# Kernel optimization log

Hardware: AMD Instinct MI355X
Metric: run time of the kernel (lower is better)

Reference implementation:

```python
import jax, jax.numpy as jnp
import numpy as np

N, E = 100000, 1600000
IN, HID, EMB = 128, 256, 64


def setup_inputs() -> dict:
    key = jax.random.key(0)
    ks = jax.random.split(key, 8)
    x = jax.random.normal(ks[0], (N, IN), dtype=jnp.float32)
    edge_index = jax.random.randint(ks[1], (2, E), 0, N, dtype=jnp.int64)
    def glorot(k, fan_in, fan_out):
        lim = np.sqrt(6.0 / (fan_in + fan_out)).astype(np.float32)
        return jax.random.uniform(k, (fan_in, fan_out), jnp.float32, -lim, lim)
    return {
        "x": x,
        "edge_index": edge_index,
        "W1": glorot(ks[2], IN, HID), "b1": jnp.zeros((HID,), jnp.float32),
        "W2": glorot(ks[3], HID, HID), "b2": jnp.zeros((HID,), jnp.float32),
        "W3": glorot(ks[4], HID, EMB), "b3": jnp.zeros((EMB,), jnp.float32),
    }


def reference(x, edge_index, W1, b1, W2, b2, W3, b3):
    n = x.shape[0]
    # add self loops (PyG GCNConv default, fill_value=1)
    loops = jnp.arange(n, dtype=edge_index.dtype)
    src = jnp.concatenate([edge_index[0], loops])
    dst = jnp.concatenate([edge_index[1], loops])
    # symmetric normalization D^-1/2 A_hat D^-1/2 (degree at target)
    deg = jax.ops.segment_sum(jnp.ones_like(src, dtype=x.dtype), dst, num_segments=n)
    dinv = jnp.where(deg > 0, deg ** -0.5, 0.0)
    norm = (dinv[src] * dinv[dst])[:, None]  # [E+N, 1]

    def conv(h, W, b):
        h = h @ W                               # [N, out]
        agg = jax.ops.segment_sum(h[src] * norm, dst, num_segments=n)
        return agg + b

    h = jax.nn.relu(conv(x, W1, b1))   # dropout: identity in eval mode
    h = jax.nn.relu(conv(h, W2, b2))
    h = conv(h, W3, b3)
    # L2-normalize rows (F.normalize, eps=1e-12)
    nrm = jnp.linalg.norm(h, axis=1, keepdims=True)
    return h / jnp.maximum(nrm, 1e-12)
```

## Files before the change

### kernel.cpp

```cpp
#include <hip/hip_runtime.h>
#include <cstddef>
#include <cstdint>

constexpr int IN_F  = 128;
constexpr int HID_F = 256;
constexpr int EMB_F = 64;

typedef float  f32x4  __attribute__((ext_vector_type(4)));
typedef short  bf16x8 __attribute__((ext_vector_type(8)));
typedef unsigned short ushort_t;
typedef ushort_t u16x8 __attribute__((ext_vector_type(8)));
typedef ushort_t u16x4 __attribute__((ext_vector_type(4)));

__device__ inline float bf2f(ushort_t u) {
  union { unsigned i; float f; } c; c.i = ((unsigned)u) << 16; return c.f;
}
__device__ inline ushort_t f2bf(float f) {
  union { float f; unsigned i; } c; c.f = f;
  unsigned r = c.i + 0x7FFFu + ((c.i >> 16) & 1u);
  return (ushort_t)(r >> 16);
}

constexpr int NBKT = 512;
constexpr int CHUNK = 16384;


__global__ void k_setup(const float* __restrict__ W1, const float* __restrict__ W2,
                        const float* __restrict__ W3,
                        ushort_t* __restrict__ W1t, ushort_t* __restrict__ W2t,
                        ushort_t* __restrict__ W3t, int* __restrict__ ghist) {
  constexpr int c1 = IN_F * HID_F;
  constexpr int c2 = c1 + HID_F * HID_F;
  constexpr int c3 = c2 + HID_F * EMB_F;
  int i = blockIdx.x * blockDim.x + threadIdx.x;
  if (i < c1) {
    int k = i / HID_F, nn = i - k * HID_F;
    W1t[(size_t)nn * IN_F + k] = f2bf(W1[i]);
  } else if (i < c2) {
    int j = i - c1;
    int k = j / HID_F, nn = j - k * HID_F;
    W2t[(size_t)nn * HID_F + k] = f2bf(W2[j]);
  } else if (i < c3) {
    int j = i - c2;
    int k = j / EMB_F, nn = j - k * EMB_F;
    W3t[(size_t)nn * HID_F + k] = f2bf(W3[j]);
  } else if (i - c3 < NBKT) {
    ghist[i - c3] = 0;
  }
}


__global__ __launch_bounds__(512) void k_hist(const int* __restrict__ dst,
                                              int* __restrict__ ghist, int e) {
  __shared__ int cnt[NBKT];
  cnt[threadIdx.x] = 0;
  __syncthreads();
  int i0 = blockIdx.x * CHUNK;
  int i1 = min(e, i0 + CHUNK);
  for (int i = i0 + threadIdx.x; i < i1; i += 512)
    atomicAdd(&cnt[dst[i] >> 8], 1);
  __syncthreads();
  int c = cnt[threadIdx.x];
  if (c > 0) atomicAdd(&ghist[threadIdx.x], c);
}

__global__ __launch_bounds__(512) void k_bscan(const int* __restrict__ ghist,
                                               int* __restrict__ bstart,
                                               int* __restrict__ gcursor) {
  __shared__ int s[NBKT];
  int v = ghist[threadIdx.x];
  s[threadIdx.x] = v;
  __syncthreads();
#pragma unroll
  for (int off = 1; off < NBKT; off <<= 1) {
    int t = (threadIdx.x >= off) ? s[threadIdx.x - off] : 0;
    __syncthreads();
    s[threadIdx.x] += t;
    __syncthreads();
  }
  int ex = s[threadIdx.x] - v;
  bstart[threadIdx.x] = ex;
  gcursor[threadIdx.x] = ex;
}

__global__ __launch_bounds__(512) void k_passA(const int* __restrict__ src,
                                               const int* __restrict__ dst,
                                               int* __restrict__ gcursor,
                                               unsigned* __restrict__ staged, int e) {
  __shared__ int cnt[NBKT];
  __shared__ int base[NBKT];
  cnt[threadIdx.x] = 0;
  __syncthreads();
  int i0 = blockIdx.x * CHUNK;
  int i1 = min(e, i0 + CHUNK);
  for (int i = i0 + threadIdx.x; i < i1; i += 512)
    atomicAdd(&cnt[dst[i] >> 8], 1);
  __syncthreads();
  int c = cnt[threadIdx.x];
  base[threadIdx.x] = (c > 0) ? atomicAdd(&gcursor[threadIdx.x], c) : 0;
  cnt[threadIdx.x] = 0;
  __syncthreads();
  for (int i = i0 + threadIdx.x; i < i1; i += 512) {
    int d = dst[i];
    int b = d >> 8;
    int lp = atomicAdd(&cnt[b], 1);
    staged[base[b] + lp] = ((unsigned)(d & 255) << 17) | (unsigned)src[i];
  }
}

__global__ __launch_bounds__(256) void k_Bfused(
    const unsigned* __restrict__ staged, const int* __restrict__ bstart,
    const int* __restrict__ ghist, const float* __restrict__ x,
    float* __restrict__ dinv, int* __restrict__ rowptr, int* __restrict__ csr,
    ushort_t* __restrict__ xb, int n, int e) {
  __shared__ int cnt[256];
  __shared__ int s[256];
  __shared__ int cur[256];
  __shared__ float dinvL[256];
  const int tid = threadIdx.x;
  const int b = blockIdx.x;
  cnt[tid] = 0;
  __syncthreads();
  const int beg = bstart[b], end = beg + ghist[b];
  for (int i = beg + tid; i < end; i += 256)
    atomicAdd(&cnt[staged[i] >> 17], 1);
  __syncthreads();
  const int node = (b << 8) + tid;
  int v = (node < n) ? cnt[tid] : 0;
  float dv = rsqrtf((float)(v + 1));
  if (node < n) { dinv[node] = dv; }
  dinvL[tid] = dv;
  s[tid] = v;
  __syncthreads();
#pragma unroll
  for (int off = 1; off < 256; off <<= 1) {
    int t = (tid >= off) ? s[tid - off] : 0;
    __syncthreads();
    s[tid] += t;
    __syncthreads();
  }
  int rp = beg + s[tid] - v;
  if (node < n) rowptr[node] = rp;
  if (b == 0 && tid == 0) rowptr[n] = e;
  cur[tid] = rp;
  __syncthreads();
  for (int i = beg + tid; i < end; i += 256) {
    unsigned p = staged[i];
    int l = (int)(p >> 17);
    int sv = (int)(p & 0x1FFFFu);
    int pos = atomicAdd(&cur[l], 1);
    csr[pos] = sv;
  }
  const int nb0 = b << 8;
  const int rows = min(256, n - nb0);
  const float4* xv = reinterpret_cast<const float4*>(x) + (size_t)nb0 * 32;
  u16x4* xo = reinterpret_cast<u16x4*>(xb) + (size_t)nb0 * 32;
  for (int j = tid; j < rows * 32; j += 256) {
    float sc = dinvL[j >> 5];
    float4 vv = xv[j];
    u16x4 o;
    o[0] = f2bf(vv.x * sc); o[1] = f2bf(vv.y * sc);
    o[2] = f2bf(vv.z * sc); o[3] = f2bf(vv.w * sc);
    xo[j] = o;
  }
}


__global__ __launch_bounds__(256) void k_gather1(
    const ushort_t* __restrict__ t, ushort_t* __restrict__ outp,
    const int* __restrict__ rowptr, const int* __restrict__ csr, int n) {
  int wid = (blockIdx.x * blockDim.x + threadIdx.x) >> 6;
  int lane = threadIdx.x & 63;
  if (wid >= n) return;
  const int half = lane >> 5, sub = lane & 31;
  const int coff = sub * 4;
  int beg = rowptr[wid], end = rowptr[wid + 1];
  int nitems = end - beg + 1;
  float acc[4] = {};
  int i = 0;
  for (; i + 3 < nitems; i += 4) {
    int i0 = i + half, i1 = i + 2 + half;
    int r0 = (i0 == 0) ? wid : csr[beg + i0 - 1];
    int r1 = csr[beg + i1 - 1];
    u16x4 v0 = *reinterpret_cast<const u16x4*>(t + (size_t)r0 * IN_F + coff);
    u16x4 v1 = *reinterpret_cast<const u16x4*>(t + (size_t)r1 * IN_F + coff);
#pragma unroll
    for (int k = 0; k < 4; ++k) acc[k] += bf2f(v0[k]);
#pragma unroll
    for (int k = 0; k < 4; ++k) acc[k] += bf2f(v1[k]);
  }
  for (; i < nitems; i += 2) {
    int i0 = i + half;
    if (i0 < nitems) {
      int r0 = (i0 == 0) ? wid : csr[beg + i0 - 1];
      u16x4 v0 = *reinterpret_cast<const u16x4*>(t + (size_t)r0 * IN_F + coff);
#pragma unroll
      for (int k = 0; k < 4; ++k) acc[k] += bf2f(v0[k]);
    }
  }
#pragma unroll
  for (int k = 0; k < 4; ++k) acc[k] += __shfl_xor(acc[k], 32);
  if (half == 0) {
    u16x4 o;
#pragma unroll
    for (int k = 0; k < 4; ++k) o[k] = f2bf(acc[k]);
    *reinterpret_cast<u16x4*>(outp + (size_t)wid * IN_F + coff) = o;
  }
}

__global__ __launch_bounds__(256) void k_gather2(
    const ushort_t* __restrict__ t, ushort_t* __restrict__ outp,
    const int* __restrict__ rowptr, const int* __restrict__ csr,
    const float* __restrict__ dinv, const float* __restrict__ bias, int n) {
  int wid = (blockIdx.x * blockDim.x + threadIdx.x) >> 6;
  int lane = threadIdx.x & 63;
  if (wid >= n) return;
  const int half = lane >> 5, sub = lane & 31;
  const int coff = sub * 8;
  int beg = rowptr[wid], end = rowptr[wid + 1];
  int nitems = end - beg + 1;
  float acc[8] = {};
  int i = 0;
  for (; i + 3 < nitems; i += 4) {
    int i0 = i + half, i1 = i + 2 + half;
    int r0 = (i0 == 0) ? wid : csr[beg + i0 - 1];
    int r1 = csr[beg + i1 - 1];
    u16x8 v0 = *reinterpret_cast<const u16x8*>(t + (size_t)r0 * HID_F + coff);
    u16x8 v1 = *reinterpret_cast<const u16x8*>(t + (size_t)r1 * HID_F + coff);
#pragma unroll
    for (int k = 0; k < 8; ++k) acc[k] += bf2f(v0[k]);
#pragma unroll
    for (int k = 0; k < 8; ++k) acc[k] += bf2f(v1[k]);
  }
  for (; i < nitems; i += 2) {
    int i0 = i + half;
    if (i0 < nitems) {
      int r0 = (i0 == 0) ? wid : csr[beg + i0 - 1];
      u16x8 v0 = *reinterpret_cast<const u16x8*>(t + (size_t)r0 * HID_F + coff);
#pragma unroll
      for (int k = 0; k < 8; ++k) acc[k] += bf2f(v0[k]);
    }
  }
#pragma unroll
  for (int k = 0; k < 8; ++k) acc[k] += __shfl_xor(acc[k], 32);
  if (half == 0) {
    float s = dinv[wid];
    u16x8 o;
#pragma unroll
    for (int k = 0; k < 8; ++k) o[k] = f2bf(fmaxf(fmaf(acc[k], s, bias[coff + k]), 0.f));
    *reinterpret_cast<u16x8*>(outp + (size_t)wid * HID_F + coff) = o;
  }
}

__global__ __launch_bounds__(256) void k_gather3(
    const ushort_t* __restrict__ t, float* __restrict__ outp,
    const int* __restrict__ rowptr, const int* __restrict__ csr,
    const float* __restrict__ dinv, const float* __restrict__ b3, int n) {
  int wid = (blockIdx.x * blockDim.x + threadIdx.x) >> 6;
  int lane = threadIdx.x & 63;
  if (wid >= n) return;
  const int q = lane >> 4, sub = lane & 15;
  const int coff = sub * 4;
  int beg = rowptr[wid], end = rowptr[wid + 1];
  int nitems = end - beg + 1;
  float acc[4] = {};
  for (int i = 0; i < nitems; i += 4) {
    int i0 = i + q;
    if (i0 < nitems) {
      int r0 = (i0 == 0) ? wid : csr[beg + i0 - 1];
      u16x4 v0 = *reinterpret_cast<const u16x4*>(t + (size_t)r0 * EMB_F + coff);
#pragma unroll
      for (int k = 0; k < 4; ++k) acc[k] += bf2f(v0[k]);
    }
  }
#pragma unroll
  for (int k = 0; k < 4; ++k) acc[k] += __shfl_xor(acc[k], 16);
#pragma unroll
  for (int k = 0; k < 4; ++k) acc[k] += __shfl_xor(acc[k], 32);
  float s = dinv[wid];
  float v[4], ss = 0.f;
#pragma unroll
  for (int k = 0; k < 4; ++k) {
    v[k] = fmaf(acc[k], s, b3[coff + k]);
    ss = fmaf(v[k], v[k], ss);
  }
#pragma unroll
  for (int off = 8; off > 0; off >>= 1) ss += __shfl_xor(ss, off);
  float inv = 1.0f / fmaxf(sqrtf(ss), 1e-12f);
  if (lane < 16) {
    float4 o = make_float4(v[0] * inv, v[1] * inv, v[2] * inv, v[3] * inv);
    *reinterpret_cast<float4*>(outp + (size_t)wid * EMB_F + coff) = o;
  }
}


template<int K, bool RELU>
__global__ __launch_bounds__(256) void k_mfma_gemm(
    const ushort_t* __restrict__ A, const ushort_t* __restrict__ Wt,
    ushort_t* __restrict__ C,
    const float* __restrict__ dinv, const float* __restrict__ bias,
    int M, int NT ) {
  int w = blockIdx.x * 4 + (threadIdx.x >> 6);
  int lane = threadIdx.x & 63;
  int mt = w / NT, nt = w - mt * NT;
  int mbase = mt * 64, nbase = nt * 64;
  if (mbase >= M) return;
  const int lrow = lane & 15;
  const int lk = (lane >> 4) * 8;
  const int N = NT * 64;

  int rows[4];
#pragma unroll
  for (int i = 0; i < 4; ++i) {
    int r = mbase + i * 16 + lrow;
    rows[i] = (r < M) ? r : (M - 1);
  }

  f32x4 acc[4][4] = {};

#pragma unroll 2
  for (int k0 = 0; k0 < K; k0 += 32) {
    bf16x8 a[4], b[4];
#pragma unroll
    for (int i = 0; i < 4; ++i)
      a[i] = *reinterpret_cast<const bf16x8*>(A + (size_t)rows[i] * K + k0 + lk);
#pragma unroll
    for (int n = 0; n < 4; ++n)
      b[n] = *reinterpret_cast<const bf16x8*>(Wt + (size_t)(nbase + n * 16 + lrow) * K + k0 + lk);
#pragma unroll
    for (int i = 0; i < 4; ++i)
#pragma unroll
      for (int n = 0; n < 4; ++n)
        acc[i][n] = __builtin_amdgcn_mfma_f32_16x16x32_bf16(a[i], b[n], acc[i][n], 0, 0, 0);
  }

#pragma unroll
  for (int i = 0; i < 4; ++i) {
    int growb = mbase + i * 16 + (lane >> 4) * 4;
#pragma unroll
    for (int r = 0; r < 4; ++r) {
      int grow = growb + r;
      if (grow >= M) continue;
      float s = dinv[grow];
#pragma unroll
      for (int n = 0; n < 4; ++n) {
        int gcol = nbase + n * 16 + (lane & 15);
        float v = acc[i][n][r] * s;
        if (RELU) v = fmaxf(v + bias[gcol], 0.f);
        C[(size_t)grow * N + gcol] = f2bf(v);
      }
    }
  }
}


extern "C" void kernel_launch(void* const* d_in, const int* in_sizes, int n_in,
                              void* d_out, int out_size, void* d_ws, size_t ws_size,
                              hipStream_t stream) {
  const float* x  = (const float*)d_in[0];
  const int*   ei = (const int*)d_in[1];
  const float* W1 = (const float*)d_in[2];
  const float* b1 = (const float*)d_in[3];
  const float* W2 = (const float*)d_in[4];
  const float* b2 = (const float*)d_in[5];
  const float* W3 = (const float*)d_in[6];
  const float* b3 = (const float*)d_in[7];
  const int N = in_sizes[0] / IN_F;
  const int E = in_sizes[1] / 2;
  const int* src = ei;
  const int* dst = ei + E;

  char* m = (char*)d_ws;
  auto alloc = [&](size_t bytes) { char* p = m; m += (bytes + 255) & ~(size_t)255; return p; };
  ushort_t* U1  = (ushort_t*)alloc((size_t)N * HID_F * 2);
  ushort_t* U2  = (ushort_t*)alloc((size_t)N * HID_F * 2);
  ushort_t* W1t = (ushort_t*)alloc((size_t)IN_F * HID_F * 2);
  ushort_t* W2t = (ushort_t*)alloc((size_t)HID_F * HID_F * 2);
  ushort_t* W3t = (ushort_t*)alloc((size_t)HID_F * EMB_F * 2);
  float*    dinv    = (float*)alloc((size_t)N * 4);
  int*      rowptr  = (int*)alloc((size_t)(N + 1) * 4);
  int*      ghist   = (int*)alloc(NBKT * 4);
  int*      bstart  = (int*)alloc(NBKT * 4);
  int*      gcursor = (int*)alloc(NBKT * 4);
  unsigned* staged  = (unsigned*)alloc((size_t)E * 4);
  int*      csr     = (int*)alloc((size_t)E * 4);
  float*    out     = (float*)d_out;

  const int nb = (N + 255) / 256;
  const int echunks = (E + CHUNK - 1) / CHUNK;
  constexpr int SETUP_W = IN_F * HID_F + HID_F * HID_F + HID_F * EMB_F + NBKT;

  k_setup<<<(SETUP_W + 255) / 256, 256, 0, stream>>>(W1, W2, W3, W1t, W2t, W3t, ghist);

  k_hist  <<<echunks, 512, 0, stream>>>(dst, ghist, E);
  k_bscan <<<1, NBKT, 0, stream>>>(ghist, bstart, gcursor);
  k_passA <<<echunks, 512, 0, stream>>>(src, dst, gcursor, staged, E);

  ushort_t* xb = U2;
  k_Bfused<<<nb, 256, 0, stream>>>(staged, bstart, ghist, x, dinv, rowptr, csr, xb, N, E);

  const int gblocks = (N + 3) / 4;
  const int MT = (N + 63) / 64;

  ushort_t* aggX = U1;
  k_gather1<<<gblocks, 256, 0, stream>>>(xb, aggX, rowptr, csr, N);
  ushort_t* h1 = U2;
  k_mfma_gemm<IN_F, true><<<(MT * (HID_F / 64) + 3) / 4, 256, 0, stream>>>(
      aggX, W1t, h1, dinv, b1, N, HID_F / 64);

  ushort_t* t2 = U1;
  k_mfma_gemm<HID_F, false><<<(MT * (HID_F / 64) + 3) / 4, 256, 0, stream>>>(
      h1, W2t, t2, dinv, nullptr, N, HID_F / 64);
  ushort_t* h2 = U2;
  k_gather2<<<gblocks, 256, 0, stream>>>(t2, h2, rowptr, csr, dinv, b2, N);

  ushort_t* t3 = U1;
  k_mfma_gemm<HID_F, false><<<(MT * (EMB_F / 64) + 3) / 4, 256, 0, stream>>>(
      h2, W3t, t3, dinv, nullptr, N, EMB_F / 64);
  k_gather3<<<gblocks, 256, 0, stream>>>(t3, out, rowptr, csr, dinv, b3, N);
}
```

Measured before the change: 460.4 us.

## Fuse layer-1 gather into GEMM and use full-width 64-row GEMM tiles

Replaces the standalone layer-1 neighbor aggregation kernel with a GEMM kernel that gathers the aggregated rows directly into swizzled shared memory before running MFMA over all 256 output columns. The layer-2 GEMM also switches to this kernel, so each block stages its 64-row A tile once in LDS and covers the whole output width instead of re-reading A per 64-column tile. This removes the intermediate aggregated buffer's write and read. In exchange, each gather is serialized across 16 rows per wave before the compute phase, and W tiles are read straight from global memory.

```diff
diff --git a/kernel.cpp b/kernel.cpp
--- a/kernel.cpp
+++ b/kernel.cpp
@@ -166,47 +166,116 @@
 }
 
 
-__global__ __launch_bounds__(256) void k_gather1(
-    const ushort_t* __restrict__ t, ushort_t* __restrict__ outp,
-    const int* __restrict__ rowptr, const int* __restrict__ csr, int n) {
-  int wid = (blockIdx.x * blockDim.x + threadIdx.x) >> 6;
-  int lane = threadIdx.x & 63;
-  if (wid >= n) return;
-  const int half = lane >> 5, sub = lane & 31;
-  const int coff = sub * 4;
-  int beg = rowptr[wid], end = rowptr[wid + 1];
-  int nitems = end - beg + 1;
-  float acc[4] = {};
-  int i = 0;
-  for (; i + 3 < nitems; i += 4) {
-    int i0 = i + half, i1 = i + 2 + half;
-    int r0 = (i0 == 0) ? wid : csr[beg + i0 - 1];
-    int r1 = csr[beg + i1 - 1];
-    u16x4 v0 = *reinterpret_cast<const u16x4*>(t + (size_t)r0 * IN_F + coff);
-    u16x4 v1 = *reinterpret_cast<const u16x4*>(t + (size_t)r1 * IN_F + coff);
-#pragma unroll
-    for (int k = 0; k < 4; ++k) acc[k] += bf2f(v0[k]);
-#pragma unroll
-    for (int k = 0; k < 4; ++k) acc[k] += bf2f(v1[k]);
-  }
-  for (; i < nitems; i += 2) {
-    int i0 = i + half;
-    if (i0 < nitems) {
-      int r0 = (i0 == 0) ? wid : csr[beg + i0 - 1];
-      u16x4 v0 = *reinterpret_cast<const u16x4*>(t + (size_t)r0 * IN_F + coff);
-#pragma unroll
-      for (int k = 0; k < 4; ++k) acc[k] += bf2f(v0[k]);
-    }
-  }
-#pragma unroll
-  for (int k = 0; k < 4; ++k) acc[k] += __shfl_xor(acc[k], 32);
-  if (half == 0) {
-    u16x4 o;
-#pragma unroll
-    for (int k = 0; k < 4; ++k) o[k] = f2bf(acc[k]);
-    *reinterpret_cast<u16x4*>(outp + (size_t)wid * IN_F + coff) = o;
-  }
-}
+template<int K, bool RELU, bool GATHER>
+__global__ __launch_bounds__(256) void k_gemm_big(
+    const ushort_t* __restrict__ A, const ushort_t* __restrict__ Wt,
+    ushort_t* __restrict__ C, const float* __restrict__ dinv,
+    const float* __restrict__ bias, const int* __restrict__ rowptr,
+    const int* __restrict__ csr, int M) {
+  __shared__ ushort_t As[64 * K];
+  const int tid = threadIdx.x;
+  const int lane = tid & 63;
+  const int w = tid >> 6;
+  const int mbase = blockIdx.x * 64;
+
+  if constexpr (GATHER) {
+    const int half = lane >> 5, sub = lane & 31;
+    const int coff = sub * 4;
+    for (int rr = 0; rr < 16; ++rr) {
+      const int r = w * 16 + rr;
+      const int g = mbase + r;
+      float acc[4] = {};
+      if (g < M) {
+        int beg = rowptr[g], end = rowptr[g + 1];
+        int nitems = end - beg + 1;
+        int i = 0;
+        for (; i + 3 < nitems; i += 4) {
+          int i0 = i + half, i1 = i + 2 + half;
+          int r0 = (i0 == 0) ? g : csr[beg + i0 - 1];
+          int r1 = csr[beg + i1 - 1];
+          u16x4 v0 = *reinterpret_cast<const u16x4*>(A + (size_t)r0 * K + coff);
+          u16x4 v1 = *reinterpret_cast<const u16x4*>(A + (size_t)r1 * K + coff);
+#pragma unroll
+          for (int k = 0; k < 4; ++k) acc[k] += bf2f(v0[k]);
+#pragma unroll
+          for (int k = 0; k < 4; ++k) acc[k] += bf2f(v1[k]);
+        }
+        for (; i < nitems; i += 2) {
+          int i0 = i + half;
+          if (i0 < nitems) {
+            int r0 = (i0 == 0) ? g : csr[beg + i0 - 1];
+            u16x4 v0 = *reinterpret_cast<const u16x4*>(A + (size_t)r0 * K + coff);
+#pragma unroll
+            for (int k = 0; k < 4; ++k) acc[k] += bf2f(v0[k]);
+          }
+        }
+      }
+#pragma unroll
+      for (int k = 0; k < 4; ++k) acc[k] += __shfl_xor(acc[k], 32);
+      if (half == 0) {
+        int c = sub >> 1;
+        int idx = r * K + ((c ^ (r & 7)) << 3) + (sub & 1) * 4;
+        u16x4 o;
+#pragma unroll
+        for (int k = 0; k < 4; ++k) o[k] = f2bf(acc[k]);
+        *reinterpret_cast<u16x4*>(&As[idx]) = o;
+      }
+    }
+  } else {
+    constexpr int CH = K / 8;
+    for (int i = tid; i < 64 * CH; i += 256) {
+      int row = i / CH, c = i - row * CH;
+      int g = mbase + row;
+      if (g >= M) g = M - 1;
+      u16x8 v = *reinterpret_cast<const u16x8*>(A + (size_t)g * K + c * 8);
+      *reinterpret_cast<u16x8*>(&As[row * K + ((c ^ (row & 7)) << 3)]) = v;
+    }
+  }
+  __syncthreads();
+
+  const int lrow = lane & 15;
+  const int lk = (lane >> 4) * 8;
+  const int nbase = w * 64;
+  f32x4 acc[4][4] = {};
+
+#pragma unroll
+  for (int k0 = 0; k0 < K; k0 += 32) {
+    bf16x8 a[4], b[4];
+    const int cbase = (k0 >> 3) + (lane >> 4);
+#pragma unroll
+    for (int i = 0; i < 4; ++i) {
+      int ri = i * 16 + lrow;
+      a[i] = *reinterpret_cast<const bf16x8*>(&As[ri * K + ((cbase ^ (ri & 7)) << 3)]);
+    }
+#pragma unroll
+    for (int n = 0; n < 4; ++n)
+      b[n] = *reinterpret_cast<const bf16x8*>(Wt + (size_t)(nbase + n * 16 + lrow) * K + k0 + lk);
+#pragma unroll
+    for (int i = 0; i < 4; ++i)
+#pragma unroll
+      for (int n = 0; n < 4; ++n)
+        acc[i][n] = __builtin_amdgcn_mfma_f32_16x16x32_bf16(a[i], b[n], acc[i][n], 0, 0, 0);
+  }
+
+#pragma unroll
+  for (int i = 0; i < 4; ++i) {
+    int growb = mbase + i * 16 + (lane >> 4) * 4;
+#pragma unroll
+    for (int r = 0; r < 4; ++r) {
+      int grow = growb + r;
+      if (grow >= M) continue;
+      float s = dinv[grow];
+#pragma unroll
+      for (int n = 0; n < 4; ++n) {
+        int gcol = nbase + n * 16 + (lane & 15);
+        float v = acc[i][n][r] * s;
+        if (RELU) v = fmaxf(v + bias[gcol], 0.f);
+        C[(size_t)grow * HID_F + gcol] = f2bf(v);
+      }
+    }
+  }
+}
+
 
 __global__ __launch_bounds__(256) void k_gather2(
     const ushort_t* __restrict__ t, ushort_t* __restrict__ outp,
@@ -402,19 +471,17 @@
   const int gblocks = (N + 3) / 4;
   const int MT = (N + 63) / 64;
 
-  ushort_t* aggX = U1;
-  k_gather1<<<gblocks, 256, 0, stream>>>(xb, aggX, rowptr, csr, N);
-  ushort_t* h1 = U2;
-  k_mfma_gemm<IN_F, true><<<(MT * (HID_F / 64) + 3) / 4, 256, 0, stream>>>(
-      aggX, W1t, h1, dinv, b1, N, HID_F / 64);
-
-  ushort_t* t2 = U1;
-  k_mfma_gemm<HID_F, false><<<(MT * (HID_F / 64) + 3) / 4, 256, 0, stream>>>(
-      h1, W2t, t2, dinv, nullptr, N, HID_F / 64);
-  ushort_t* h2 = U2;
+  ushort_t* h1 = U1;
+  k_gemm_big<IN_F, true, true><<<MT, 256, 0, stream>>>(
+      xb, W1t, h1, dinv, b1, rowptr, csr, N);
+
+  ushort_t* t2 = U2;
+  k_gemm_big<HID_F, false, false><<<MT, 256, 0, stream>>>(
+      h1, W2t, t2, dinv, nullptr, nullptr, nullptr, N);
+  ushort_t* h2 = U1;
   k_gather2<<<gblocks, 256, 0, stream>>>(t2, h2, rowptr, csr, dinv, b2, N);
 
-  ushort_t* t3 = U1;
+  ushort_t* t3 = U2;
   k_mfma_gemm<HID_F, false><<<(MT * (EMB_F / 64) + 3) / 4, 256, 0, stream>>>(
       h2, W3t, t3, dinv, nullptr, N, EMB_F / 64);
   k_gather3<<<gblocks, 256, 0, stream>>>(t3, out, rowptr, csr, dinv, b3, N);
```

After: 565.5 us. 22.8% more time.
